# Performance work log

Measured on AMD Instinct MI355X. Metric: run time of the kernel, lower is better.

The kernel has to match this reference:

```python
import jax, jax.numpy as jnp
import numpy as np
from math import sqrt

GAMMA = 2.0       # init gamma
SIGMA_G = 1.0     # init sigma (Gaussian prior width) -- NOT the forward `sigma` arg
ALPHA = 0.1       # prior mixing weight


def _hilbert_filter(L, dtype):
    h = np.zeros(L, dtype=np.float32)
    if L % 2 == 0:
        h[0] = h[L // 2] = 1.0
        h[1:L // 2] = 2.0
    else:
        h[0] = 1.0
        h[1:(L + 1) // 2] = 2.0
    return jnp.asarray(h)


def setup_inputs() -> dict:
    key = jax.random.key(0)
    ks = jax.random.split(key, 6)
    B, L, H, E = 4, 1024, 8, 64
    return {
        "q": jax.random.normal(ks[0], (B, L, H, E), jnp.float32),
        "k": jax.random.normal(ks[1], (B, L, H, E), jnp.float32),
        "v": jax.random.normal(ks[2], (B, L, H, E), jnp.float32),
        "sigma": jax.random.normal(ks[3], (B, L, H), jnp.float32),
        "hurst": jax.random.normal(ks[4], (B, L, H), jnpp if False else jnp.float32) if False else jax.random.normal(ks[4], (B, L, H), jnp.float32),
        "tau": jax.random.normal(ks[5], (B, L, H), jnp.float32),
    }


def reference(q, k, v, sigma, hurst, tau):
    B, L, H, E = q.shape
    scale = 1.0 / sqrt(E)

    # QK scores [B,H,L,L]. Note: original calls scores.masked_fill (non-inplace,
    # result discarded), so the causal mask has NO effect -- reproduced faithfully.
    scores = jnp.einsum('blhe,bshe->bhls', q, k)
    attn = scale * scores

    hurst_t = jax.nn.sigmoid(hurst) * 0.99 + 0.01          # [B,L,H]
    tau_t = jax.nn.sigmoid(tau) * 0.9 + 0.1                # [B,L,H]

    # fractal abscissa -> Gaussian prior [B,H,L,L]
    psi = jnp.cumsum(jnp.exp(GAMMA * hurst_t), axis=1)     # [B,L,H]
    diff = psi[:, :, None, :] - psi[:, None, :, :]          # [B,L,L,H]
    prior = jnp.exp(-diff ** 2 / (2.0 * SIGMA_G ** 2))
    prior = jnp.transpose(prior, (0, 3, 1, 2))              # [B,H,L,L]
    prior = prior / (jnp.sum(prior, axis=-1, keepdims=True) + 1e-6)

    # phase gate from Hilbert analytic signal of q-features
    x = jnp.transpose(q, (0, 2, 1, 3)).reshape(B, L, H * E)  # [B,L,C]
    sig = jnp.transpose(x, (0, 2, 1))                         # [B,C,L]
    hfilt = _hilbert_filter(L, sig.dtype)
    analytic = jnp.fft.ifft(jnp.fft.fft(sig, axis=-1) * hfilt[None, None, :], axis=-1)
    phase = jnp.arctan2(jnp.imag(analytic), jnp.real(analytic))  # [B,C,L]
    theta = jnp.arctan2(jnp.mean(jnp.sin(phase), axis=1),
                        jnp.mean(jnp.cos(phase), axis=1))        # [B,L]
    dphi = jnp.sin(0.5 * (theta[:, :, None] - theta[:, None, :]))  # [B,L,L]
    tau_d = jax.lax.stop_gradient(tau_t)                     # tau is detached
    S = jnp.exp(-dphi[..., None] ** 2 / (2.0 * tau_d[:, :, None, :] ** 2))  # [B,L,L,H]
    gate = jnp.transpose(S, (0, 3, 1, 2))                    # [B,H,L,L]

    prior = prior * gate
    prior = prior / (jnp.sum(prior, axis=-1, keepdims=True) + 1e-6)

    series = jax.nn.softmax(attn, axis=-1)                   # dropout p=0
    attn_combined = (1.0 - ALPHA) * series + ALPHA * prior
    V = jnp.einsum('bhls,bshd->blhd', attn_combined, v)      # [B,L,H,E]
    return V
```

## Files before the change

### kernel.cpp

```cpp
#include <hip/hip_runtime.h>
#include <hip/hip_bf16.h>
#include <math.h>

#define LL 1024
#define BB 4
#define HH 8
#define EE 64
#define CC (HH*EE)

typedef __attribute__((ext_vector_type(4))) float f32x4;
typedef __attribute__((ext_vector_type(8))) short bf16x8;
typedef __attribute__((ext_vector_type(4))) short bf16x4;

__device__ __forceinline__ unsigned short f2bf(float x) {
    unsigned u = __float_as_uint(x);
    u += 0x7FFFu + ((u >> 16) & 1u);
    return (unsigned short)(u >> 16);
}

__device__ __forceinline__ void dma16(const void* g, void* l) {
    typedef const __attribute__((address_space(1))) unsigned int* gup;
    typedef __attribute__((address_space(3))) unsigned int* lup;
    gup gp = (gup)(unsigned long long)g;
    lup lp = (lup)(unsigned int)(unsigned long long)l;
    __builtin_amdgcn_global_load_lds(gp, lp, 16, 0, 0);
}

__global__ __launch_bounds__(1024) void k_pre(const float* __restrict__ hurst,
                                              const float* __restrict__ tau,
                                              const float* __restrict__ q,
                                              float* __restrict__ psi,
                                              float* __restrict__ taut,
                                              unsigned short* __restrict__ Agh,
                                              unsigned short* __restrict__ Agl,
                                              unsigned short* __restrict__ Xh,
                                              unsigned short* __restrict__ Xl) {
    __shared__ float sh[1024];
    int bid = blockIdx.x;
    int t = threadIdx.x;

    if (bid < 32) {
        int bh = bid;
        int b = bh >> 3, h = bh & 7;
        int l = t;
        float hu = hurst[((size_t)b * LL + l) * HH + h];
        float ht = 1.f / (1.f + expf(-hu)) * 0.99f + 0.01f;
        sh[l] = expf(2.0f * ht);
        __syncthreads();
        for (int off = 1; off < LL; off <<= 1) {
            float tmp = (l >= off) ? sh[l - off] : 0.f;
            __syncthreads();
            sh[l] += tmp;
            __syncthreads();
        }
        psi[((size_t)b * HH + h) * LL + l] = sh[l];
        float tv = tau[((size_t)b * LL + l) * HH + h];
        taut[((size_t)b * HH + h) * LL + l] = 1.f / (1.f + expf(-tv)) * 0.9f + 0.1f;
    } else if (bid < 288) {
        {
            int d = t;
            float vv = 0.f;
            if (d & 1) {
                float a = 3.14159265358979323846f * (float)d / (float)LL;
                vv = (2.0f / (float)LL) * (cosf(a) / sinf(a));
            }
            sh[d] = vv;
        }
        __syncthreads();
        int bb = bid - 32;
        int im = bb >> 4, kt = bb & 15;
        if (t < 512) {
            int row = t >> 3, gr = t & 7;
            int i = im * 64 + row;
            bf16x8 hv, lv;
            #pragma unroll
            for (int j = 0; j < 8; ++j) {
                int kl = gr * 8 + j;
                float gg = sh[(i - kt * 64 - kl) & 1023];
                unsigned short hh = f2bf(gg);
                hv[j] = (short)hh;
                lv[j] = (short)f2bf(gg - __uint_as_float(((unsigned)hh) << 16));
            }
            size_t base = (size_t)bb * 4096;
            int pos = gr ^ (row & 7);
            *(bf16x8*)&Agh[base + row * 64 + pos * 8] = hv;
            *(bf16x8*)&Agl[base + row * 64 + pos * 8] = lv;
        }
    } else {
        int bb = bid - 288;
        int kt = bb >> 4, np = bb & 15;
        int bq = np >> 2;
        const float* qb = q + (size_t)bq * LL * CC;
        size_t base = (size_t)bb * 8192;
        int gid = t;
        int nl = gid & 15, nb = (gid >> 4) & 7, kg = gid >> 7;
        int e_n = np * 128 + nb * 16 + nl;
        int cy = (e_n >> 6) & 7;
        int e = e_n & 63;
        bf16x8 hv, lv;
        #pragma unroll
        for (int j = 0; j < 8; ++j) {
            int k = kt * 64 + kg * 8 + j;
            int l = ((k & 127) << 3) | cy;
            int h2 = k >> 7;
            float val = qb[l * 512 + h2 * 64 + e];
            unsigned short hh = f2bf(val);
            hv[j] = (short)hh;
            lv[j] = (short)f2bf(val - __uint_as_float(((unsigned)hh) << 16));
        }
        *(bf16x8*)&Xh[base + (size_t)gid * 8] = hv;
        *(bf16x8*)&Xl[base + (size_t)gid * 8] = lv;
    }
}

__global__ __launch_bounds__(256) void k_hilb(const float* __restrict__ q,
                                              const unsigned short* __restrict__ Agh,
                                              const unsigned short* __restrict__ Agl,
                                              const unsigned short* __restrict__ Xh,
                                              const unsigned short* __restrict__ Xl,
                                              float* __restrict__ part_s,
                                              float* __restrict__ part_c) {
    __shared__ __align__(16) char smemB[98304];

    int t = threadIdx.x, lid = t & 63, wv = t >> 6;
    int m16 = lid & 15, g = lid >> 4;
    int wi = wv >> 1, wn = wv & 1;

    int bid = blockIdx.x;
    int xcd = bid & 7, o = bid >> 3;
    int im = ((xcd >> 2) << 3) + (o & 7);
    int np = ((xcd & 3) << 2) + (o >> 3);
    int i0 = im * 64, n0 = np * 128;
    int bq = np >> 2, quad = np & 3;
    const float* qb = q + (size_t)bq * LL * CC;

    const char* Ah_g = (const char*)Agh + (size_t)im * 16 * 8192;
    const char* Al_g = (const char*)Agl + (size_t)im * 16 * 8192;
    const char* Xh_g = (const char*)Xh;
    const char* Xl_g = (const char*)Xl;

#define AHOFF(bf) ((bf) * 49152)
#define ALOFF(bf) ((bf) * 49152 + 8192)
#define XHOFF(bf) ((bf) * 49152 + 16384)
#define XLOFF(bf) ((bf) * 49152 + 32768)
#define STAGE(bf, kt)                                                          \
    {                                                                          \
        size_t xb = ((size_t)(kt) * 16 + np) * 16384;                          \
        _Pragma("unroll")                                                      \
        for (int c = 0; c < 2; ++c) {                                          \
            int ch = wv + 4 * c;                                               \
            dma16(Ah_g + (kt) * 8192 + ch * 1024 + lid * 16,                   \
                  smemB + AHOFF(bf) + ch * 1024);                              \
            dma16(Al_g + (kt) * 8192 + ch * 1024 + lid * 16,                   \
                  smemB + ALOFF(bf) + ch * 1024);                              \
        }                                                                      \
        _Pragma("unroll")                                                      \
        for (int c = 0; c < 4; ++c) {                                          \
            int ch = wv + 4 * c;                                               \
            dma16(Xh_g + xb + ch * 1024 + lid * 16,                            \
                  smemB + XHOFF(bf) + ch * 1024);                              \
            dma16(Xl_g + xb + ch * 1024 + lid * 16,                            \
                  smemB + XLOFF(bf) + ch * 1024);                              \
        }                                                                      \
    }

    STAGE(0, 0);
    __syncthreads();

    f32x4 acc[2][4];
    #pragma unroll
    for (int mf = 0; mf < 2; ++mf)
        #pragma unroll
        for (int nf = 0; nf < 4; ++nf) acc[mf][nf] = (f32x4){0.f, 0.f, 0.f, 0.f};

    int cur = 0;
    for (int kt = 0; kt < 16; ++kt) {
        if (kt < 15) STAGE(cur ^ 1, kt + 1);

        const unsigned short* AhL = (const unsigned short*)(smemB + AHOFF(cur));
        const unsigned short* AlL = (const unsigned short*)(smemB + ALOFF(cur));
        const unsigned short* XhL = (const unsigned short*)(smemB + XHOFF(cur));
        const unsigned short* XlL = (const unsigned short*)(smemB + XLOFF(cur));

        #pragma unroll
        for (int s = 0; s < 2; ++s) {
            bf16x8 Ahf[2], Alf[2];
            #pragma unroll
            for (int mf = 0; mf < 2; ++mf) {
                int row = wi * 32 + 16 * mf + m16;
                int pos = (s * 4 + g) ^ (m16 & 7);
                Ahf[mf] = *(bf16x8*)&AhL[row * 64 + pos * 8];
                Alf[mf] = *(bf16x8*)&AlL[row * 64 + pos * 8];
            }
            #pragma unroll
            for (int nf = 0; nf < 4; ++nf) {
                int nb = wn * 4 + nf;
                int goff = (((s * 4 + g) * 8 + nb) * 16 + m16) * 8;
                bf16x8 Bh = *(bf16x8*)&XhL[goff];
                bf16x8 Bl = *(bf16x8*)&XlL[goff];
                #pragma unroll
                for (int mf = 0; mf < 2; ++mf) {
                    acc[mf][nf] = __builtin_amdgcn_mfma_f32_16x16x32_bf16(Ahf[mf], Bh, acc[mf][nf], 0, 0, 0);
                    acc[mf][nf] = __builtin_amdgcn_mfma_f32_16x16x32_bf16(Ahf[mf], Bl, acc[mf][nf], 0, 0, 0);
                    acc[mf][nf] = __builtin_amdgcn_mfma_f32_16x16x32_bf16(Alf[mf], Bh, acc[mf][nf], 0, 0, 0);
                }
            }
        }
        __syncthreads();
        cur ^= 1;
    }

    float svacc[2][4], cvacc[2][4];
    #pragma unroll
    for (int mf = 0; mf < 2; ++mf)
        #pragma unroll
        for (int r = 0; r < 4; ++r) { svacc[mf][r] = 0.f; cvacc[mf][r] = 0.f; }

    #pragma unroll
    for (int mf = 0; mf < 2; ++mf) {
        #pragma unroll
        for (int nf = 0; nf < 4; ++nf) {
            #pragma unroll
            for (int r = 0; r < 4; ++r) {
                float iv = acc[mf][nf][r];
                int ig = i0 + wi * 32 + 16 * mf + 4 * g + r;
                int ng = n0 + wn * 64 + 16 * nf + m16;
                int cc2 = ng & 511;
                int cy = cc2 >> 6, e = cc2 & 63;
                int l = ((ig & 127) << 3) | cy;
                int h2 = ig >> 7;
                float re = qb[l * 512 + h2 * 64 + e];
                float rr = sqrtf(re * re + iv * iv);
                float sv, cv;
                if (rr > 0.f) { sv = iv / rr; cv = re / rr; }
                else { sv = 0.f; cv = 1.f; }
                svacc[mf][r] += sv;
                cvacc[mf][r] += cv;
            }
        }
    }
    float* psv = (float*)smemB;
    float* pcv = (float*)(smemB + 512);
    #pragma unroll
    for (int mf = 0; mf < 2; ++mf) {
        #pragma unroll
        for (int r = 0; r < 4; ++r) {
            float s = svacc[mf][r], c = cvacc[mf][r];
            s += __shfl_xor(s, 1); s += __shfl_xor(s, 2);
            s += __shfl_xor(s, 4); s += __shfl_xor(s, 8);
            c += __shfl_xor(c, 1); c += __shfl_xor(c, 2);
            c += __shfl_xor(c, 4); c += __shfl_xor(c, 8);
            if (m16 == 0) {
                psv[wv * 32 + 16 * mf + 4 * g + r] = s;
                pcv[wv * 32 + 16 * mf + 4 * g + r] = c;
            }
        }
    }
    __syncthreads();
    if (t < 64) {
        int wg = (t >> 5) * 2;
        float s = psv[wg * 32 + (t & 31)] + psv[(wg + 1) * 32 + (t & 31)];
        float c = pcv[wg * 32 + (t & 31)] + pcv[(wg + 1) * 32 + (t & 31)];
        size_t oidx = ((size_t)bq * 1024 + (i0 + t)) * 4 + quad;
        part_s[oidx] = s;
        part_c[oidx] = c;
    }
#undef AHOFF
#undef ALOFF
#undef XHOFF
#undef XLOFF
#undef STAGE
}

__global__ __launch_bounds__(256) void k_prep(const float* __restrict__ q,
                                              const float* __restrict__ k,
                                              const float* __restrict__ v,
                                              const float* __restrict__ psi,
                                              const float* __restrict__ taut,
                                              const float* __restrict__ part_s,
                                              const float* __restrict__ part_c,
                                              unsigned short* __restrict__ Qp,
                                              unsigned short* __restrict__ Kp,
                                              unsigned short* __restrict__ Vp,
                                              float* __restrict__ pcs) {
    __shared__ unsigned short vt[4096];
    int t = threadIdx.x;
    int blk = blockIdx.x;
    int tile = blk & 15;
    int bh = blk >> 4;
    int h = bh & 7, b = bh >> 3;
    int l0 = tile * 64;

    const float* qg = q + ((size_t)(b * LL + l0) * CC + (size_t)h * EE);
    const float* kg = k + ((size_t)(b * LL + l0) * CC + (size_t)h * EE);
    const float* vg = v + ((size_t)(b * LL + l0) * CC + (size_t)h * EE);
    unsigned short* Qo = Qp + ((size_t)bh * LL + l0) * 64;
    unsigned short* Ko = Kp + ((size_t)bh * LL + l0) * 64;
    unsigned short* Vo = Vp + ((size_t)bh * 16 + tile) * 4096;

    const float QS = 0.18033688011112042f;

    #pragma unroll
    for (int it = 0; it < 2; ++it) {
        int x = it * 256 + t;
        int row = x >> 3, gr = x & 7;
        int pos = (gr ^ (row & 7)) * 8;
        const float* src = qg + (size_t)row * CC + gr * 8;
        float4 a4 = *(const float4*)src;
        float4 b4 = *(const float4*)(src + 4);
        bf16x8 o;
        o[0] = (short)f2bf(QS * a4.x); o[1] = (short)f2bf(QS * a4.y);
        o[2] = (short)f2bf(QS * a4.z); o[3] = (short)f2bf(QS * a4.w);
        o[4] = (short)f2bf(QS * b4.x); o[5] = (short)f2bf(QS * b4.y);
        o[6] = (short)f2bf(QS * b4.z); o[7] = (short)f2bf(QS * b4.w);
        *(bf16x8*)&Qo[row * 64 + pos] = o;
        src = kg + (size_t)row * CC + gr * 8;
        a4 = *(const float4*)src;
        b4 = *(const float4*)(src + 4);
        o[0] = (short)f2bf(a4.x); o[1] = (short)f2bf(a4.y);
        o[2] = (short)f2bf(a4.z); o[3] = (short)f2bf(a4.w);
        o[4] = (short)f2bf(b4.x); o[5] = (short)f2bf(b4.y);
        o[6] = (short)f2bf(b4.z); o[7] = (short)f2bf(b4.w);
        *(bf16x8*)&Ko[row * 64 + pos] = o;
    }

    #pragma unroll
    for (int it = 0; it < 4; ++it) {
        int x = it * 256 + t;
        int s = x >> 4, i = x & 15;
        float4 a4 = *(const float4*)(vg + (size_t)s * CC + i * 4);
        int c = s >> 5, g4 = (s >> 2) & 3;
        int jj = ((s >> 4) & 1) * 4 + (s & 3);
        float vals[4] = {a4.x, a4.y, a4.z, a4.w};
        #pragma unroll
        for (int j2 = 0; j2 < 4; ++j2) {
            int e = i * 4 + j2;
            int ef = e >> 4, m16 = e & 15;
            vt[((((ef * 2 + c) * 4 + g4) * 16 + m16) * 8) + jj] = f2bf(vals[j2]);
        }
    }
    __syncthreads();
    #pragma unroll
    for (int it = 0; it < 2; ++it) {
        int x = it * 256 + t;
        *(bf16x8*)&Vo[x * 8] = *(bf16x8*)&vt[x * 8];
    }

    if (t < 64) {
        int l = l0 + t;
        float ss = 0.f, cc2 = 0.f;
        size_t pbase = ((size_t)b * 1024 + l) * 4;
        #pragma unroll
        for (int qd = 0; qd < 4; ++qd) {
            ss += part_s[pbase + qd];
            cc2 += part_c[pbase + qd];
        }
        float r2 = ss * ss + cc2 * cc2;
        float cth = 1.f, sth = 0.f;
        if (r2 > 0.f) {
            float rn = rsqrtf(r2);
            cth = cc2 * rn; sth = ss * rn;
        }
        float ta = taut[(size_t)bh * LL + l];
        float4 o;
        o.x = psi[(size_t)bh * LL + l] * 0.8493218003f;
        o.y = cth;
        o.z = sth;
        o.w = 0.3606737602f / (ta * ta);
        *(float4*)&pcs[((size_t)bh * LL + l) * 4] = o;
    }
}

__global__ __launch_bounds__(256, 3) void k_attn(const unsigned short* __restrict__ Qp,
                                                 const unsigned short* __restrict__ Kp,
                                                 const unsigned short* __restrict__ Vp,
                                                 const float* __restrict__ pcs,
                                                 float* __restrict__ out) {
    __shared__ __align__(16) char smemB[43008];

    int t = threadIdx.x;
    int lid = t & 63;
    int wv = t >> 6;
    int m16 = lid & 15;
    int g = lid >> 4;

    int bid = blockIdx.x;
    int blk = (bid & 7) * 64 + (bid >> 3);
    int qt = blk & 15;
    int bh = blk >> 4;
    int h = bh & 7, b = bh >> 3;
    int l0 = qt * 64;

    const char* Qg = (const char*)(Qp + ((size_t)bh * LL + l0) * 64);
    const char* Kg = (const char*)(Kp + (size_t)bh * LL * 64);
    const char* Vg = (const char*)(Vp + (size_t)bh * LL * 64);
    const float* pcsg = pcs + (size_t)bh * LL * 4;

    int qrow = wv * 16 + m16;
    float4 myq = *(const float4*)&pcsg[(size_t)(l0 + qrow) * 4];
    float psiq = myq.x, cq = myq.y, sq = myq.z;
    float wgt = myq.w, nwgt = -myq.w;

#define KOFF(bf) (8192 + (bf) * 8192)
#define VOFF(bf) (24576 + (bf) * 8192)
#define POFF(bf) (40960 + (bf) * 1024)
#define STAGE(bf, tile)                                                        \
    {                                                                          \
        const char* kb8 = Kg + (tile) * 8192;                                  \
        const char* vb8 = Vg + (tile) * 8192;                                  \
        _Pragma("unroll")                                                      \
        for (int c = 0; c < 2; ++c) {                                          \
            int ch = wv + 4 * c;                                               \
            dma16(kb8 + ch * 1024 + lid * 16, smemB + KOFF(bf) + ch * 1024);   \
            dma16(vb8 + ch * 1024 + lid * 16, smemB + VOFF(bf) + ch * 1024);   \
        }                                                                      \
        dma16((const char*)pcsg + (tile) * 1024 + lid * 16, smemB + POFF(bf)); \
    }

    #pragma unroll
    for (int c = 0; c < 2; ++c) {
        int ch = wv + 4 * c;
        dma16(Qg + ch * 1024 + lid * 16, smemB + ch * 1024);
    }
    STAGE(0, 0);
    __syncthreads();

    const unsigned short* qlds = (const unsigned short*)smemB;
    bf16x8 qf[2];
    #pragma unroll
    for (int ec = 0; ec < 2; ++ec) {
        int pos = (4 * ec + g) ^ (m16 & 7);
        qf[ec] = *(bf16x8*)&qlds[(wv * 16 + m16) * 64 + pos * 8];
    }

    f32x4 accS[4], accP[4];
    #pragma unroll
    for (int f = 0; f < 4; ++f) {
        accS[f] = (f32x4){0.f, 0.f, 0.f, 0.f};
        accP[f] = (f32x4){0.f, 0.f, 0.f, 0.f};
    }
    float ssel = 0.f, spgl = 0.f;
    int cur = 0;

    for (int tile = 0; tile < 16; ++tile) {
        if (tile < 15) {
            STAGE(cur ^ 1, tile + 1);
            asm volatile("s_waitcnt vmcnt(5)" ::: "memory");
        } else {
            asm volatile("s_waitcnt vmcnt(0)" ::: "memory");
        }
        __builtin_amdgcn_sched_barrier(0);
        __builtin_amdgcn_s_barrier();
        asm volatile("" ::: "memory");

        const unsigned short* kbuf = (const unsigned short*)(smemB + KOFF(cur));
        const unsigned short* vbuf = (const unsigned short*)(smemB + VOFF(cur));
        const float* pcb = (const float*)(smemB + POFF(cur));

        f32x4 st[4];
        #pragma unroll
        for (int f = 0; f < 4; ++f) st[f] = (f32x4){0.f, 0.f, 0.f, 0.f};
        __builtin_amdgcn_s_setprio(1);
        #pragma unroll
        for (int ec = 0; ec < 2; ++ec) {
            int pos = (4 * ec + g) ^ (m16 & 7);
            #pragma unroll
            for (int f = 0; f < 4; ++f) {
                bf16x8 ka = *(bf16x8*)&kbuf[(16 * f + m16) * 64 + pos * 8];
                st[f] = __builtin_amdgcn_mfma_f32_16x16x32_bf16(ka, qf[ec], st[f], 0, 0, 0);
            }
        }
        __builtin_amdgcn_s_setprio(0);

        float psum = 0.f;
        float ps_[16], pg_[16];
        #pragma unroll
        for (int f = 0; f < 4; ++f) {
            #pragma unroll
            for (int r = 0; r < 4; ++r) {
                float4 pc4 = *(const float4*)&pcb[(16 * f + 4 * g + r) * 4];
                float p = exp2f(st[f][r]);
                psum += p;
                float d = psiq - pc4.x;
                float cd = fmaf(cq, pc4.y, sq * pc4.z);
                float arg = fmaf(-d, d, fmaf(wgt, cd, nwgt));
                float pgv = exp2f(arg);
                spgl += pgv;
                ps_[f * 4 + r] = p;
                pg_[f * 4 + r] = pgv;
            }
        }
        ssel += psum;

        union PK8 { unsigned w[8]; bf16x8 v[2]; } SS, GG;
        #pragma unroll
        for (int i2 = 0; i2 < 8; ++i2) {
            __hip_bfloat162 hs = __float22bfloat162_rn(
                make_float2(ps_[2 * i2], ps_[2 * i2 + 1]));
            __hip_bfloat162 hg = __float22bfloat162_rn(
                make_float2(pg_[2 * i2], pg_[2 * i2 + 1]));
            unsigned ws, wg2;
            __builtin_memcpy(&ws, &hs, 4);
            __builtin_memcpy(&wg2, &hg, 4);
            SS.w[i2] = ws;
            GG.w[i2] = wg2;
        }

        __builtin_amdgcn_s_setprio(1);
        #pragma unroll
        for (int c = 0; c < 2; ++c) {
            #pragma unroll
            for (int ef = 0; ef < 4; ++ef) {
                bf16x8 vb = *(bf16x8*)&vbuf[(((ef * 2 + c) * 4 + g) * 16 + m16) * 8];
                accS[ef] = __builtin_amdgcn_mfma_f32_16x16x32_bf16(SS.v[c], vb, accS[ef], 0, 0, 0);
                accP[ef] = __builtin_amdgcn_mfma_f32_16x16x32_bf16(GG.v[c], vb, accP[ef], 0, 0, 0);
            }
        }
        __builtin_amdgcn_s_setprio(0);

        asm volatile("" ::: "memory");
        __builtin_amdgcn_s_barrier();
        cur ^= 1;
    }

    ssel += __shfl_xor(ssel, 16); ssel += __shfl_xor(ssel, 32);
    spgl += __shfl_xor(spgl, 16); spgl += __shfl_xor(spgl, 32);
    float cs = 0.9f / ssel;
    float cp = 0.1f / (spgl + 1e-6f);
    float* ob = out + ((size_t)(b * LL + l0 + wv * 16) * CC + (size_t)h * EE);
    #pragma unroll
    for (int r = 0; r < 4; ++r) {
        float csr = __shfl(cs, 4 * g + r);
        float cpr = __shfl(cp, 4 * g + r);
        #pragma unroll
        for (int f = 0; f < 4; ++f) {
            ob[(size_t)(4 * g + r) * CC + 16 * f + m16] =
                csr * accS[f][r] + cpr * accP[f][r];
        }
    }
#undef KOFF
#undef VOFF
#undef POFF
#undef STAGE
}

extern "C" void kernel_launch(void* const* d_in, const int* in_sizes, int n_in,
                              void* d_out, int out_size, void* d_ws, size_t ws_size,
                              hipStream_t stream) {
    const float* q = (const float*)d_in[0];
    const float* k = (const float*)d_in[1];
    const float* v = (const float*)d_in[2];
    const float* hurst = (const float*)d_in[4];
    const float* tau = (const float*)d_in[5];
    float* out = (float*)d_out;

    float* ws = (float*)d_ws;
    float* gi     = ws;
    float* psi    = gi + LL;
    float* taut   = psi + (size_t)BB * HH * LL;
    float* costh  = taut + (size_t)BB * HH * LL;
    float* sinth  = costh + (size_t)BB * LL;
    float* part_s = sinth + (size_t)BB * LL;
    float* part_c = part_s + (size_t)BB * LL * 4;
    float* pcs    = part_c + (size_t)BB * LL * 4;
    unsigned short* Qp = (unsigned short*)(pcs + (size_t)BB * HH * LL * 4);
    unsigned short* Kp = Qp + (size_t)BB * HH * LL * 64;
    unsigned short* Vp = Kp + (size_t)BB * HH * LL * 64;

    unsigned short* Agh = Qp;
    unsigned short* Agl = Qp + (size_t)1048576;
    unsigned short* Xh  = Kp;
    unsigned short* Xl  = Vp;

    k_pre<<<544, 1024, 0, stream>>>(hurst, tau, q, psi, taut, Agh, Agl, Xh, Xl);
    k_hilb<<<256, 256, 0, stream>>>(q, Agh, Agl, Xh, Xl, part_s, part_c);
    k_prep<<<BB * HH * 16, 256, 0, stream>>>(q, k, v, psi, taut, part_s, part_c,
                                             Qp, Kp, Vp, pcs);
    k_attn<<<BB * HH * (LL / 64), 256, 0, stream>>>(Qp, Kp, Vp, pcs, out);
}
```

Baseline: 82.38 us.

## Split attention key tiles across two wave groups and pipeline the Hilbert GEMM loop

The attention kernel now runs 512 threads per block. Two groups of four waves each handle half of every 64-key tile, and their partial accumulators and row sums are combined through shared memory at the end. Q fragments are loaded straight from global memory rather than staged through LDS, which shrinks the LDS footprint. The Hilbert GEMM loop swaps __syncthreads for explicit vmcnt waits, raw barriers and setprio, so the next tile's DMA can overlap compute. The cost is an extra cross-group reduction and more pressure on the register and wave budget per CU.

```diff
diff --git a/kernel.cpp b/kernel.cpp
--- a/kernel.cpp
+++ b/kernel.cpp
@@ -175,13 +175,22 @@
 
     int cur = 0;
     for (int kt = 0; kt < 16; ++kt) {
-        if (kt < 15) STAGE(cur ^ 1, kt + 1);
+        if (kt < 15) {
+            STAGE(cur ^ 1, kt + 1);
+            asm volatile("s_waitcnt vmcnt(12)" ::: "memory");
+        } else {
+            asm volatile("s_waitcnt vmcnt(0)" ::: "memory");
+        }
+        __builtin_amdgcn_sched_barrier(0);
+        __builtin_amdgcn_s_barrier();
+        asm volatile("" ::: "memory");
 
         const unsigned short* AhL = (const unsigned short*)(smemB + AHOFF(cur));
         const unsigned short* AlL = (const unsigned short*)(smemB + ALOFF(cur));
         const unsigned short* XhL = (const unsigned short*)(smemB + XHOFF(cur));
         const unsigned short* XlL = (const unsigned short*)(smemB + XLOFF(cur));
 
+        __builtin_amdgcn_s_setprio(1);
         #pragma unroll
         for (int s = 0; s < 2; ++s) {
             bf16x8 Ahf[2], Alf[2];
@@ -206,7 +215,10 @@
                 }
             }
         }
-        __syncthreads();
+        __builtin_amdgcn_s_setprio(0);
+
+        asm volatile("" ::: "memory");
+        __builtin_amdgcn_s_barrier();
         cur ^= 1;
     }
 
@@ -239,6 +251,7 @@
             }
         }
     }
+    __syncthreads();
     float* psv = (float*)smemB;
     float* pcv = (float*)(smemB + 512);
     #pragma unroll
@@ -371,16 +384,17 @@
     }
 }
 
-__global__ __launch_bounds__(256, 3) void k_attn(const unsigned short* __restrict__ Qp,
+__global__ __launch_bounds__(512, 4) void k_attn(const unsigned short* __restrict__ Qp,
                                                  const unsigned short* __restrict__ Kp,
                                                  const unsigned short* __restrict__ Vp,
                                                  const float* __restrict__ pcs,
                                                  float* __restrict__ out) {
-    __shared__ __align__(16) char smemB[43008];
+    __shared__ __align__(16) char smemB[35840];
 
     int t = threadIdx.x;
     int lid = t & 63;
     int wv = t >> 6;
+    int qg = wv & 3, sg = wv >> 2;
     int m16 = lid & 15;
     int g = lid >> 4;
 
@@ -396,42 +410,31 @@
     const char* Vg = (const char*)(Vp + (size_t)bh * LL * 64);
     const float* pcsg = pcs + (size_t)bh * LL * 4;
 
-    int qrow = wv * 16 + m16;
+    int qrow = qg * 16 + m16;
     float4 myq = *(const float4*)&pcsg[(size_t)(l0 + qrow) * 4];
     float psiq = myq.x, cq = myq.y, sq = myq.z;
     float wgt = myq.w, nwgt = -myq.w;
 
-#define KOFF(bf) (8192 + (bf) * 8192)
-#define VOFF(bf) (24576 + (bf) * 8192)
-#define POFF(bf) (40960 + (bf) * 1024)
+#define KOFF(bf) ((bf) * 8192)
+#define VOFF(bf) (16384 + (bf) * 8192)
+#define POFF(bf) (32768 + (bf) * 1024)
 #define STAGE(bf, tile)                                                        \
     {                                                                          \
         const char* kb8 = Kg + (tile) * 8192;                                  \
         const char* vb8 = Vg + (tile) * 8192;                                  \
-        _Pragma("unroll")                                                      \
-        for (int c = 0; c < 2; ++c) {                                          \
-            int ch = wv + 4 * c;                                               \
-            dma16(kb8 + ch * 1024 + lid * 16, smemB + KOFF(bf) + ch * 1024);   \
-            dma16(vb8 + ch * 1024 + lid * 16, smemB + VOFF(bf) + ch * 1024);   \
-        }                                                                      \
+        dma16(kb8 + wv * 1024 + lid * 16, smemB + KOFF(bf) + wv * 1024);       \
+        dma16(vb8 + wv * 1024 + lid * 16, smemB + VOFF(bf) + wv * 1024);       \
         dma16((const char*)pcsg + (tile) * 1024 + lid * 16, smemB + POFF(bf)); \
     }
 
-    #pragma unroll
-    for (int c = 0; c < 2; ++c) {
-        int ch = wv + 4 * c;
-        dma16(Qg + ch * 1024 + lid * 16, smemB + ch * 1024);
+    bf16x8 qf[2];
+    #pragma unroll
+    for (int ec = 0; ec < 2; ++ec) {
+        int pos = (4 * ec + g) ^ (m16 & 7);
+        qf[ec] = *(const bf16x8*)(Qg + ((qg * 16 + m16) * 64 + pos * 8) * 2);
     }
     STAGE(0, 0);
     __syncthreads();
-
-    const unsigned short* qlds = (const unsigned short*)smemB;
-    bf16x8 qf[2];
-    #pragma unroll
-    for (int ec = 0; ec < 2; ++ec) {
-        int pos = (4 * ec + g) ^ (m16 & 7);
-        qf[ec] = *(bf16x8*)&qlds[(wv * 16 + m16) * 64 + pos * 8];
-    }
 
     f32x4 accS[4], accP[4];
     #pragma unroll
@@ -445,7 +448,7 @@
     for (int tile = 0; tile < 16; ++tile) {
         if (tile < 15) {
             STAGE(cur ^ 1, tile + 1);
-            asm volatile("s_waitcnt vmcnt(5)" ::: "memory");
+            asm volatile("s_waitcnt vmcnt(3)" ::: "memory");
         } else {
             asm volatile("s_waitcnt vmcnt(0)" ::: "memory");
         }
@@ -457,28 +460,28 @@
         const unsigned short* vbuf = (const unsigned short*)(smemB + VOFF(cur));
         const float* pcb = (const float*)(smemB + POFF(cur));
 
-        f32x4 st[4];
-        #pragma unroll
-        for (int f = 0; f < 4; ++f) st[f] = (f32x4){0.f, 0.f, 0.f, 0.f};
+        f32x4 st[2];
+        st[0] = (f32x4){0.f, 0.f, 0.f, 0.f};
+        st[1] = (f32x4){0.f, 0.f, 0.f, 0.f};
         __builtin_amdgcn_s_setprio(1);
         #pragma unroll
         for (int ec = 0; ec < 2; ++ec) {
             int pos = (4 * ec + g) ^ (m16 & 7);
             #pragma unroll
-            for (int f = 0; f < 4; ++f) {
-                bf16x8 ka = *(bf16x8*)&kbuf[(16 * f + m16) * 64 + pos * 8];
+            for (int f = 0; f < 2; ++f) {
+                bf16x8 ka = *(bf16x8*)&kbuf[(sg * 32 + 16 * f + m16) * 64 + pos * 8];
                 st[f] = __builtin_amdgcn_mfma_f32_16x16x32_bf16(ka, qf[ec], st[f], 0, 0, 0);
             }
         }
         __builtin_amdgcn_s_setprio(0);
 
         float psum = 0.f;
-        float ps_[16], pg_[16];
-        #pragma unroll
-        for (int f = 0; f < 4; ++f) {
+        float ps_[8], pg_[8];
+        #pragma unroll
+        for (int f = 0; f < 2; ++f) {
             #pragma unroll
             for (int r = 0; r < 4; ++r) {
-                float4 pc4 = *(const float4*)&pcb[(16 * f + 4 * g + r) * 4];
+                float4 pc4 = *(const float4*)&pcb[(sg * 32 + 16 * f + 4 * g + r) * 4];
                 float p = exp2f(st[f][r]);
                 psum += p;
                 float d = psiq - pc4.x;
@@ -492,9 +495,9 @@
         }
         ssel += psum;
 
-        union PK8 { unsigned w[8]; bf16x8 v[2]; } SS, GG;
-        #pragma unroll
-        for (int i2 = 0; i2 < 8; ++i2) {
+        union PK4 { unsigned w[4]; bf16x8 v; } SS, GG;
+        #pragma unroll
+        for (int i2 = 0; i2 < 4; ++i2) {
             __hip_bfloat162 hs = __float22bfloat162_rn(
                 make_float2(ps_[2 * i2], ps_[2 * i2 + 1]));
             __hip_bfloat162 hg = __float22bfloat162_rn(
@@ -508,13 +511,10 @@
 
         __builtin_amdgcn_s_setprio(1);
         #pragma unroll
-        for (int c = 0; c < 2; ++c) {
-            #pragma unroll
-            for (int ef = 0; ef < 4; ++ef) {
-                bf16x8 vb = *(bf16x8*)&vbuf[(((ef * 2 + c) * 4 + g) * 16 + m16) * 8];
-                accS[ef] = __builtin_amdgcn_mfma_f32_16x16x32_bf16(SS.v[c], vb, accS[ef], 0, 0, 0);
-                accP[ef] = __builtin_amdgcn_mfma_f32_16x16x32_bf16(GG.v[c], vb, accP[ef], 0, 0, 0);
-            }
+        for (int ef = 0; ef < 4; ++ef) {
+            bf16x8 vb = *(bf16x8*)&vbuf[(((ef * 2 + sg) * 4 + g) * 16 + m16) * 8];
+            accS[ef] = __builtin_amdgcn_mfma_f32_16x16x32_bf16(SS.v, vb, accS[ef], 0, 0, 0);
+            accP[ef] = __builtin_amdgcn_mfma_f32_16x16x32_bf16(GG.v, vb, accP[ef], 0, 0, 0);
         }
         __builtin_amdgcn_s_setprio(0);
 
@@ -525,17 +525,45 @@
 
     ssel += __shfl_xor(ssel, 16); ssel += __shfl_xor(ssel, 32);
     spgl += __shfl_xor(spgl, 16); spgl += __shfl_xor(spgl, 32);
-    float cs = 0.9f / ssel;
-    float cp = 0.1f / (spgl + 1e-6f);
-    float* ob = out + ((size_t)(b * LL + l0 + wv * 16) * CC + (size_t)h * EE);
-    #pragma unroll
-    for (int r = 0; r < 4; ++r) {
-        float csr = __shfl(cs, 4 * g + r);
-        float cpr = __shfl(cp, 4 * g + r);
+
+    float* red = (float*)smemB;
+    int rbase = (qg * 64 + lid) * 35;
+    if (sg == 1) {
         #pragma unroll
         for (int f = 0; f < 4; ++f) {
-            ob[(size_t)(4 * g + r) * CC + 16 * f + m16] =
-                csr * accS[f][r] + cpr * accP[f][r];
+            *(f32x4*)&red[rbase + f * 4] = accS[f];
+            *(f32x4*)&red[rbase + 16 + f * 4] = accP[f];
+        }
+        red[rbase + 32] = ssel;
+        red[rbase + 33] = spgl;
+    }
+    __syncthreads();
+    if (sg == 0) {
+        #pragma unroll
+        for (int f = 0; f < 4; ++f) {
+            f32x4 aS = *(f32x4*)&red[rbase + f * 4];
+            f32x4 aP = *(f32x4*)&red[rbase + 16 + f * 4];
+            #pragma unroll
+            for (int r = 0; r < 4; ++r) {
+                accS[f][r] += aS[r];
+                accP[f][r] += aP[r];
+            }
+        }
+        ssel += red[rbase + 32];
+        spgl += red[rbase + 33];
+
+        float cs = 0.9f / ssel;
+        float cp = 0.1f / (spgl + 1e-6f);
+        float* ob = out + ((size_t)(b * LL + l0 + qg * 16) * CC + (size_t)h * EE);
+        #pragma unroll
+        for (int r = 0; r < 4; ++r) {
+            float csr = __shfl(cs, 4 * g + r);
+            float cpr = __shfl(cp, 4 * g + r);
+            #pragma unroll
+            for (int f = 0; f < 4; ++f) {
+                ob[(size_t)(4 * g + r) * CC + 16 * f + m16] =
+                    csr * accS[f][r] + cpr * accP[f][r];
+            }
         }
     }
 #undef KOFF
@@ -576,5 +604,5 @@
     k_hilb<<<256, 256, 0, stream>>>(q, Agh, Agl, Xh, Xl, part_s, part_c);
     k_prep<<<BB * HH * 16, 256, 0, stream>>>(q, k, v, psi, taut, part_s, part_c,
                                              Qp, Kp, Vp, pcs);
-    k_attn<<<BB * HH * (LL / 64), 256, 0, stream>>>(Qp, Kp, Vp, pcs, out);
+    k_attn<<<BB * HH * (LL / 64), 512, 0, stream>>>(Qp, Kp, Vp, pcs, out);
 }
```

After: 83.19 us. Within noise of the previous version (+1.0%).

## Move Q/K/V bf16 packing into pre-kernel and pipeline Hilbert GEMM staging

Applied to the files above, without the earlier changes.

The Q/K/V bf16 conversion and V transposition move from the post-Hilbert prep kernel into the first pre-kernel as 128 extra blocks, so this work runs alongside the other preprocessing instead of after the Hilbert GEMM. The leftover pcs computation becomes a small separate kernel. Scratch buffers are relocated so the Hilbert operands no longer alias Qp/Kp/Vp, with Xh/Xl placed in the output buffer. The Hilbert loop replaces __syncthreads with explicit vmcnt waits, raw barriers and setprio to overlap the DMA prefetch with MFMA work, at the cost of a fourth kernel launch and more fragile hand-written synchronisation.

```diff
diff --git a/kernel.cpp b/kernel.cpp
--- a/kernel.cpp
+++ b/kernel.cpp
@@ -26,20 +26,26 @@
     __builtin_amdgcn_global_load_lds(gp, lp, 16, 0, 0);
 }
 
-__global__ __launch_bounds__(1024) void k_pre(const float* __restrict__ hurst,
-                                              const float* __restrict__ tau,
-                                              const float* __restrict__ q,
-                                              float* __restrict__ psi,
-                                              float* __restrict__ taut,
-                                              unsigned short* __restrict__ Agh,
-                                              unsigned short* __restrict__ Agl,
-                                              unsigned short* __restrict__ Xh,
-                                              unsigned short* __restrict__ Xl) {
-    __shared__ float sh[1024];
+__global__ __launch_bounds__(1024) void k_pre1(const float* __restrict__ hurst,
+                                               const float* __restrict__ tau,
+                                               const float* __restrict__ q,
+                                               const float* __restrict__ kk,
+                                               const float* __restrict__ vv,
+                                               float* __restrict__ psi,
+                                               float* __restrict__ taut,
+                                               unsigned short* __restrict__ Agh,
+                                               unsigned short* __restrict__ Agl,
+                                               unsigned short* __restrict__ Xh,
+                                               unsigned short* __restrict__ Xl,
+                                               unsigned short* __restrict__ Qp,
+                                               unsigned short* __restrict__ Kp,
+                                               unsigned short* __restrict__ Vp) {
+    __shared__ __align__(16) char smem[32768];
     int bid = blockIdx.x;
     int t = threadIdx.x;
 
     if (bid < 32) {
+        float* sh = (float*)smem;
         int bh = bid;
         int b = bh >> 3, h = bh & 7;
         int l = t;
@@ -57,14 +63,15 @@
         float tv = tau[((size_t)b * LL + l) * HH + h];
         taut[((size_t)b * HH + h) * LL + l] = 1.f / (1.f + expf(-tv)) * 0.9f + 0.1f;
     } else if (bid < 288) {
+        float* sh = (float*)smem;
         {
             int d = t;
-            float vv = 0.f;
+            float vvv = 0.f;
             if (d & 1) {
                 float a = 3.14159265358979323846f * (float)d / (float)LL;
-                vv = (2.0f / (float)LL) * (cosf(a) / sinf(a));
-            }
-            sh[d] = vv;
+                vvv = (2.0f / (float)LL) * (cosf(a) / sinf(a));
+            }
+            sh[d] = vvv;
         }
         __syncthreads();
         int bb = bid - 32;
@@ -86,7 +93,7 @@
             *(bf16x8*)&Agh[base + row * 64 + pos * 8] = hv;
             *(bf16x8*)&Agl[base + row * 64 + pos * 8] = lv;
         }
-    } else {
+    } else if (bid < 544) {
         int bb = bid - 288;
         int kt = bb >> 4, np = bb & 15;
         int bq = np >> 2;
@@ -100,9 +107,9 @@
         bf16x8 hv, lv;
         #pragma unroll
         for (int j = 0; j < 8; ++j) {
-            int k = kt * 64 + kg * 8 + j;
-            int l = ((k & 127) << 3) | cy;
-            int h2 = k >> 7;
+            int k2 = kt * 64 + kg * 8 + j;
+            int l = ((k2 & 127) << 3) | cy;
+            int h2 = k2 >> 7;
             float val = qb[l * 512 + h2 * 64 + e];
             unsigned short hh = f2bf(val);
             hv[j] = (short)hh;
@@ -110,6 +117,70 @@
         }
         *(bf16x8*)&Xh[base + (size_t)gid * 8] = hv;
         *(bf16x8*)&Xl[base + (size_t)gid * 8] = lv;
+    } else {
+        int bb = bid - 544;
+        int sub = t >> 8, tt = t & 255;
+        int blk = bb * 4 + sub;
+        int tile = blk & 15;
+        int bh = blk >> 4;
+        int h = bh & 7, b = bh >> 3;
+        int l0 = tile * 64;
+        unsigned short* vt = (unsigned short*)smem + sub * 4096;
+
+        const float* qg = q + ((size_t)(b * LL + l0) * CC + (size_t)h * EE);
+        const float* kg = kk + ((size_t)(b * LL + l0) * CC + (size_t)h * EE);
+        const float* vg = vv + ((size_t)(b * LL + l0) * CC + (size_t)h * EE);
+        unsigned short* Qo = Qp + ((size_t)bh * LL + l0) * 64;
+        unsigned short* Ko = Kp + ((size_t)bh * LL + l0) * 64;
+        unsigned short* Vo = Vp + ((size_t)bh * 16 + tile) * 4096;
+
+        const float QS = 0.18033688011112042f;
+
+        #pragma unroll
+        for (int it = 0; it < 2; ++it) {
+            int x = it * 256 + tt;
+            int row = x >> 3, gr = x & 7;
+            int pos = (gr ^ (row & 7)) * 8;
+            const float* src = qg + (size_t)row * CC + gr * 8;
+            float4 a4 = *(const float4*)src;
+            float4 b4 = *(const float4*)(src + 4);
+            bf16x8 o;
+            o[0] = (short)f2bf(QS * a4.x); o[1] = (short)f2bf(QS * a4.y);
+            o[2] = (short)f2bf(QS * a4.z); o[3] = (short)f2bf(QS * a4.w);
+            o[4] = (short)f2bf(QS * b4.x); o[5] = (short)f2bf(QS * b4.y);
+            o[6] = (short)f2bf(QS * b4.z); o[7] = (short)f2bf(QS * b4.w);
+            *(bf16x8*)&Qo[row * 64 + pos] = o;
+            src = kg + (size_t)row * CC + gr * 8;
+            a4 = *(const float4*)src;
+            b4 = *(const float4*)(src + 4);
+            o[0] = (short)f2bf(a4.x); o[1] = (short)f2bf(a4.y);
+            o[2] = (short)f2bf(a4.z); o[3] = (short)f2bf(a4.w);
+            o[4] = (short)f2bf(b4.x); o[5] = (short)f2bf(b4.y);
+            o[6] = (short)f2bf(b4.z); o[7] = (short)f2bf(b4.w);
+            *(bf16x8*)&Ko[row * 64 + pos] = o;
+        }
+
+        #pragma unroll
+        for (int it = 0; it < 4; ++it) {
+            int x = it * 256 + tt;
+            int s = x >> 4, i = x & 15;
+            float4 a4 = *(const float4*)(vg + (size_t)s * CC + i * 4);
+            int c = s >> 5, g4 = (s >> 2) & 3;
+            int jj = ((s >> 4) & 1) * 4 + (s & 3);
+            float vals[4] = {a4.x, a4.y, a4.z, a4.w};
+            #pragma unroll
+            for (int j2 = 0; j2 < 4; ++j2) {
+                int e = i * 4 + j2;
+                int ef = e >> 4, m16 = e & 15;
+                vt[((((ef * 2 + c) * 4 + g4) * 16 + m16) * 8) + jj] = f2bf(vals[j2]);
+            }
+        }
+        __syncthreads();
+        #pragma unroll
+        for (int it = 0; it < 2; ++it) {
+            int x = it * 256 + tt;
+            *(bf16x8*)&Vo[x * 8] = *(bf16x8*)&vt[x * 8];
+        }
     }
 }
 
@@ -175,13 +246,22 @@
 
     int cur = 0;
     for (int kt = 0; kt < 16; ++kt) {
-        if (kt < 15) STAGE(cur ^ 1, kt + 1);
+        if (kt < 15) {
+            STAGE(cur ^ 1, kt + 1);
+            asm volatile("s_waitcnt vmcnt(12)" ::: "memory");
+        } else {
+            asm volatile("s_waitcnt vmcnt(0)" ::: "memory");
+        }
+        __builtin_amdgcn_sched_barrier(0);
+        __builtin_amdgcn_s_barrier();
+        asm volatile("" ::: "memory");
 
         const unsigned short* AhL = (const unsigned short*)(smemB + AHOFF(cur));
         const unsigned short* AlL = (const unsigned short*)(smemB + ALOFF(cur));
         const unsigned short* XhL = (const unsigned short*)(smemB + XHOFF(cur));
         const unsigned short* XlL = (const unsigned short*)(smemB + XLOFF(cur));
 
+        __builtin_amdgcn_s_setprio(1);
         #pragma unroll
         for (int s = 0; s < 2; ++s) {
             bf16x8 Ahf[2], Alf[2];
@@ -206,7 +286,10 @@
                 }
             }
         }
-        __syncthreads();
+        __builtin_amdgcn_s_setprio(0);
+
+        asm volatile("" ::: "memory");
+        __builtin_amdgcn_s_barrier();
         cur ^= 1;
     }
 
@@ -239,6 +322,7 @@
             }
         }
     }
+    __syncthreads();
     float* psv = (float*)smemB;
     float* pcv = (float*)(smemB + 512);
     #pragma unroll
@@ -272,103 +356,34 @@
 #undef STAGE
 }
 
-__global__ __launch_bounds__(256) void k_prep(const float* __restrict__ q,
-                                              const float* __restrict__ k,
-                                              const float* __restrict__ v,
-                                              const float* __restrict__ psi,
+__global__ __launch_bounds__(1024) void k_pcs(const float* __restrict__ psi,
                                               const float* __restrict__ taut,
                                               const float* __restrict__ part_s,
                                               const float* __restrict__ part_c,
-                                              unsigned short* __restrict__ Qp,
-                                              unsigned short* __restrict__ Kp,
-                                              unsigned short* __restrict__ Vp,
                                               float* __restrict__ pcs) {
-    __shared__ unsigned short vt[4096];
-    int t = threadIdx.x;
-    int blk = blockIdx.x;
-    int tile = blk & 15;
-    int bh = blk >> 4;
-    int h = bh & 7, b = bh >> 3;
-    int l0 = tile * 64;
-
-    const float* qg = q + ((size_t)(b * LL + l0) * CC + (size_t)h * EE);
-    const float* kg = k + ((size_t)(b * LL + l0) * CC + (size_t)h * EE);
-    const float* vg = v + ((size_t)(b * LL + l0) * CC + (size_t)h * EE);
-    unsigned short* Qo = Qp + ((size_t)bh * LL + l0) * 64;
-    unsigned short* Ko = Kp + ((size_t)bh * LL + l0) * 64;
-    unsigned short* Vo = Vp + ((size_t)bh * 16 + tile) * 4096;
-
-    const float QS = 0.18033688011112042f;
-
-    #pragma unroll
-    for (int it = 0; it < 2; ++it) {
-        int x = it * 256 + t;
-        int row = x >> 3, gr = x & 7;
-        int pos = (gr ^ (row & 7)) * 8;
-        const float* src = qg + (size_t)row * CC + gr * 8;
-        float4 a4 = *(const float4*)src;
-        float4 b4 = *(const float4*)(src + 4);
-        bf16x8 o;
-        o[0] = (short)f2bf(QS * a4.x); o[1] = (short)f2bf(QS * a4.y);
-        o[2] = (short)f2bf(QS * a4.z); o[3] = (short)f2bf(QS * a4.w);
-        o[4] = (short)f2bf(QS * b4.x); o[5] = (short)f2bf(QS * b4.y);
-        o[6] = (short)f2bf(QS * b4.z); o[7] = (short)f2bf(QS * b4.w);
-        *(bf16x8*)&Qo[row * 64 + pos] = o;
-        src = kg + (size_t)row * CC + gr * 8;
-        a4 = *(const float4*)src;
-        b4 = *(const float4*)(src + 4);
-        o[0] = (short)f2bf(a4.x); o[1] = (short)f2bf(a4.y);
-        o[2] = (short)f2bf(a4.z); o[3] = (short)f2bf(a4.w);
-        o[4] = (short)f2bf(b4.x); o[5] = (short)f2bf(b4.y);
-        o[6] = (short)f2bf(b4.z); o[7] = (short)f2bf(b4.w);
-        *(bf16x8*)&Ko[row * 64 + pos] = o;
-    }
-
-    #pragma unroll
-    for (int it = 0; it < 4; ++it) {
-        int x = it * 256 + t;
-        int s = x >> 4, i = x & 15;
-        float4 a4 = *(const float4*)(vg + (size_t)s * CC + i * 4);
-        int c = s >> 5, g4 = (s >> 2) & 3;
-        int jj = ((s >> 4) & 1) * 4 + (s & 3);
-        float vals[4] = {a4.x, a4.y, a4.z, a4.w};
-        #pragma unroll
-        for (int j2 = 0; j2 < 4; ++j2) {
-            int e = i * 4 + j2;
-            int ef = e >> 4, m16 = e & 15;
-            vt[((((ef * 2 + c) * 4 + g4) * 16 + m16) * 8) + jj] = f2bf(vals[j2]);
-        }
-    }
-    __syncthreads();
-    #pragma unroll
-    for (int it = 0; it < 2; ++it) {
-        int x = it * 256 + t;
-        *(bf16x8*)&Vo[x * 8] = *(bf16x8*)&vt[x * 8];
-    }
-
-    if (t < 64) {
-        int l = l0 + t;
-        float ss = 0.f, cc2 = 0.f;
-        size_t pbase = ((size_t)b * 1024 + l) * 4;
-        #pragma unroll
-        for (int qd = 0; qd < 4; ++qd) {
-            ss += part_s[pbase + qd];
-            cc2 += part_c[pbase + qd];
-        }
-        float r2 = ss * ss + cc2 * cc2;
-        float cth = 1.f, sth = 0.f;
-        if (r2 > 0.f) {
-            float rn = rsqrtf(r2);
-            cth = cc2 * rn; sth = ss * rn;
-        }
-        float ta = taut[(size_t)bh * LL + l];
-        float4 o;
-        o.x = psi[(size_t)bh * LL + l] * 0.8493218003f;
-        o.y = cth;
-        o.z = sth;
-        o.w = 0.3606737602f / (ta * ta);
-        *(float4*)&pcs[((size_t)bh * LL + l) * 4] = o;
-    }
+    int tid = blockIdx.x * 1024 + threadIdx.x;
+    int bh = tid >> 10, l = tid & 1023;
+    int b = bh >> 3;
+    float ss = 0.f, cc2 = 0.f;
+    size_t pbase = ((size_t)b * 1024 + l) * 4;
+    #pragma unroll
+    for (int qd = 0; qd < 4; ++qd) {
+        ss += part_s[pbase + qd];
+        cc2 += part_c[pbase + qd];
+    }
+    float r2 = ss * ss + cc2 * cc2;
+    float cth = 1.f, sth = 0.f;
+    if (r2 > 0.f) {
+        float rn = rsqrtf(r2);
+        cth = cc2 * rn; sth = ss * rn;
+    }
+    float ta = taut[tid];
+    float4 o;
+    o.x = psi[tid] * 0.8493218003f;
+    o.y = cth;
+    o.z = sth;
+    o.w = 0.3606737602f / (ta * ta);
+    *(float4*)&pcs[(size_t)tid * 4] = o;
 }
 
 __global__ __launch_bounds__(256, 3) void k_attn(const unsigned short* __restrict__ Qp,
@@ -499,10 +514,10 @@
                 make_float2(ps_[2 * i2], ps_[2 * i2 + 1]));
             __hip_bfloat162 hg = __float22bfloat162_rn(
                 make_float2(pg_[2 * i2], pg_[2 * i2 + 1]));
-            unsigned ws, wg2;
-            __builtin_memcpy(&ws, &hs, 4);
+            unsigned ws2, wg2;
+            __builtin_memcpy(&ws2, &hs, 4);
             __builtin_memcpy(&wg2, &hg, 4);
-            SS.w[i2] = ws;
+            SS.w[i2] = ws2;
             GG.w[i2] = wg2;
         }
 
@@ -566,15 +581,14 @@
     unsigned short* Qp = (unsigned short*)(pcs + (size_t)BB * HH * LL * 4);
     unsigned short* Kp = Qp + (size_t)BB * HH * LL * 64;
     unsigned short* Vp = Kp + (size_t)BB * HH * LL * 64;
-
-    unsigned short* Agh = Qp;
-    unsigned short* Agl = Qp + (size_t)1048576;
-    unsigned short* Xh  = Kp;
-    unsigned short* Xl  = Vp;
-
-    k_pre<<<544, 1024, 0, stream>>>(hurst, tau, q, psi, taut, Agh, Agl, Xh, Xl);
+    unsigned short* Agh = Vp + (size_t)BB * HH * LL * 64;
+    unsigned short* Agl = Agh + (size_t)1048576;
+    unsigned short* Xh  = (unsigned short*)d_out;
+    unsigned short* Xl  = Xh + (size_t)2097152;
+
+    k_pre1<<<672, 1024, 0, stream>>>(hurst, tau, q, k, v, psi, taut,
+                                     Agh, Agl, Xh, Xl, Qp, Kp, Vp);
     k_hilb<<<256, 256, 0, stream>>>(q, Agh, Agl, Xh, Xl, part_s, part_c);
-    k_prep<<<BB * HH * 16, 256, 0, stream>>>(q, k, v, psi, taut, part_s, part_c,
-                                             Qp, Kp, Vp, pcs);
+    k_pcs<<<32, 1024, 0, stream>>>(psi, taut, part_s, part_c, pcs);
     k_attn<<<BB * HH * (LL / 64), 256, 0, stream>>>(Qp, Kp, Vp, pcs, out);
 }
```

Result: faster. 80.32 us (-2.5%).
